# Performance work log

Measured on AMD Instinct MI355X. Metric: run time of the kernel, lower is better.

Reference implementation:

```python
import jax, jax.numpy as jnp
import numpy as np

HEADS = 16
DIM_HEAD = 64
LN_EPS = 1e-5


def _layernorm(x, gamma, beta):
    mu = jnp.mean(x, axis=-1, keepdims=True)
    var = jnp.mean(jnp.square(x - mu), axis=-1, keepdims=True)
    return (x - mu) * jax.lax.rsqrt(var + LN_EPS) * gamma + beta


def setup_inputs() -> dict:
    key = jax.random.key(0)
    k1, k2, k3 = jax.random.split(key, 3)
    B, N, D = 4, 2048, 1024
    inner = HEADS * DIM_HEAD  # 1024
    x = jax.random.normal(k1, (B, N, D), dtype=jnp.float32)
    ln_gamma = jnp.ones((D,), dtype=jnp.float32)
    ln_beta = jnp.zeros((D,), dtype=jnp.float32)
    w_qkv = jax.random.normal(k2, (3 * inner, D), dtype=jnp.float32) * (1.0 / np.sqrt(D))
    w_out = jax.random.normal(k3, (D, inner), dtype=jnp.float32) * (1.0 / np.sqrt(inner))
    b_out = jnp.zeros((D,), dtype=jnp.float32)
    return {"x": x, "ln_gamma": ln_gamma, "ln_beta": ln_beta,
            "w_qkv": w_qkv, "w_out": w_out, "b_out": b_out}


def reference(x, ln_gamma, ln_beta, w_qkv, w_out, b_out):
    B, N, D = x.shape
    h, d = HEADS, DIM_HEAD
    xn = _layernorm(x, ln_gamma, ln_beta)
    qkv = xn @ w_qkv.T  # [B, N, 3*inner]
    q, k, v = jnp.split(qkv, 3, axis=-1)
    q = q.reshape(B, N, h, d)
    k = k.reshape(B, N, h, d)
    v = v.reshape(B, N, h, d)
    scale = 1.0 / np.sqrt(d)  # TET uses 1/sqrt(E); tau=1, delta=0, no mask
    scores = jnp.einsum('blhe,bshe->bhls', q, k)
    A = jax.nn.softmax(scale * scores, axis=-1)  # [B, H, N, N]
    out = jnp.einsum('bhls,bshd->blhd', A, v).reshape(B, N, h * d)
    return out @ w_out.T + b_out
```

## Files before the change

kernel.cpp:

```cpp
#include <hip/hip_runtime.h>

typedef unsigned short ushortT;
typedef __attribute__((ext_vector_type(8))) short short8;
typedef __attribute__((ext_vector_type(4))) float f32x4;

#define QSCALE 0.18033688011112042f

__device__ __forceinline__ ushortT f2bf(float f) {
  union { float f; unsigned int u; } v; v.f = f;
  unsigned int r = v.u + 0x7FFFu + ((v.u >> 16) & 1u);
  return (ushortT)(r >> 16);
}

__device__ __forceinline__ unsigned int pk2bf(float a, float b) {
  union { float f; unsigned int u; } ua, ub; ua.f = a; ub.f = b;
  return __builtin_amdgcn_perm(ub.u + 0x8000u, ua.u + 0x8000u, 0x07060302u);
}

__device__ __forceinline__ void pl_swap(unsigned int& a, unsigned int& b) {
  asm("v_permlane32_swap_b32 %0, %1" : "+v"(a), "+v"(b));
  asm("v_permlane16_swap_b32 %0, %1" : "+v"(a), "+v"(b));
}

__device__ __forceinline__ void gld_lds16(const void* g, void* l) {
  __builtin_amdgcn_global_load_lds(
      (const __attribute__((address_space(1))) unsigned int*)g,
      (__attribute__((address_space(3))) unsigned int*)l, 16, 0, 0);
}

__global__ __launch_bounds__(256) void cvt_kernel(const float* __restrict__ src,
                                                  ushortT* __restrict__ dst, int n4) {
  int i = blockIdx.x * 256 + threadIdx.x;
  if (i < n4) {
    float4 v = ((const float4*)src)[i];
    ushort4 o;
    o.x = f2bf(v.x); o.y = f2bf(v.y); o.z = f2bf(v.z); o.w = f2bf(v.w);
    ((ushort4*)dst)[i] = o;
  }
}

__global__ __launch_bounds__(256) void ln_kernel(const float* __restrict__ x,
                                                 const float* __restrict__ g,
                                                 const float* __restrict__ be,
                                                 ushortT* __restrict__ xn) {
  const int row = blockIdx.x, tid = threadIdx.x;
  const float4 v = ((const float4*)(x + (size_t)row * 1024))[tid];
  float s1 = v.x + v.y + v.z + v.w;
  float s2 = v.x * v.x + v.y * v.y + v.z * v.z + v.w * v.w;
#pragma unroll
  for (int off = 32; off >= 1; off >>= 1) {
    s1 += __shfl_xor(s1, off, 64);
    s2 += __shfl_xor(s2, off, 64);
  }
  __shared__ float red[8];
  const int wave = tid >> 6, lane = tid & 63;
  if (lane == 0) { red[wave] = s1; red[4 + wave] = s2; }
  __syncthreads();
  s1 = red[0] + red[1] + red[2] + red[3];
  s2 = red[4] + red[5] + red[6] + red[7];
  const float mean = s1 * (1.0f / 1024.0f);
  const float var  = s2 * (1.0f / 1024.0f) - mean * mean;
  const float rs = rsqrtf(var + 1e-5f);
  const float4 gv = ((const float4*)g)[tid];
  const float4 bv = ((const float4*)be)[tid];
  ushort4 o;
  o.x = f2bf((v.x - mean) * rs * gv.x + bv.x);
  o.y = f2bf((v.y - mean) * rs * gv.y + bv.y);
  o.z = f2bf((v.z - mean) * rs * gv.z + bv.z);
  o.w = f2bf((v.w - mean) * rs * gv.w + bv.w);
  ((ushort4*)xn)[(size_t)row * 256 + tid] = o;
}

template <int MODE>
__global__ __launch_bounds__(256, 2) void gemm_bt(
    const ushortT* __restrict__ A, const ushortT* __restrict__ Bm,
    int M, int N, int K,
    ushortT* __restrict__ qbuf, ushortT* __restrict__ kbuf, ushortT* __restrict__ vbuf,
    float* __restrict__ outf, const float* __restrict__ bias) {
  __shared__ ushortT lds_a[128 * 64];
  __shared__ ushortT lds_b[128 * 64];
  const int tid = threadIdx.x;
  const int wave = tid >> 6, lane = tid & 63;
  const int q4 = lane >> 4, l16 = lane & 15;
  const int m0 = blockIdx.y * 128, n0 = blockIdx.x * 128;
  const int wm = (wave >> 1) * 64, wn = (wave & 1) * 64;
  const int srow = lane >> 3, scol = (lane & 7) * 8;

  f32x4 acc[4][4];
#pragma unroll
  for (int i = 0; i < 4; i++)
#pragma unroll
    for (int j = 0; j < 4; j++) acc[i][j] = (f32x4){0.f, 0.f, 0.f, 0.f};

  for (int k0 = 0; k0 < K; k0 += 64) {
#pragma unroll
    for (int j = 0; j < 4; j++) {
      const int q = wave * 4 + j;
      gld_lds16(&A[(size_t)(m0 + q * 8 + srow) * K + (k0 + scol)], &lds_a[q * 512]);
      gld_lds16(&Bm[(size_t)(n0 + q * 8 + srow) * K + (k0 + scol)], &lds_b[q * 512]);
    }
    __syncthreads();
#pragma unroll
    for (int kk = 0; kk < 2; kk++) {
      short8 af[4], bf[4];
#pragma unroll
      for (int i = 0; i < 4; i++)
        af[i] = *(const short8*)&lds_a[(wm + i * 16 + l16) * 64 + kk * 32 + q4 * 8];
#pragma unroll
      for (int i = 0; i < 4; i++)
        bf[i] = *(const short8*)&lds_b[(wn + i * 16 + l16) * 64 + kk * 32 + q4 * 8];
#pragma unroll
      for (int im = 0; im < 4; im++)
#pragma unroll
        for (int in = 0; in < 4; in++)
          acc[im][in] = __builtin_amdgcn_mfma_f32_16x16x32_bf16(af[im], bf[in], acc[im][in], 0, 0, 0);
    }
    __syncthreads();
  }

#pragma unroll
  for (int im = 0; im < 4; im++) {
    const int grow_base = m0 + wm + im * 16 + q4 * 4;
#pragma unroll
    for (int in = 0; in < 4; in++) {
      const int c = n0 + wn + in * 16 + l16;
#pragma unroll
      for (int r = 0; r < 4; r++) {
        const float v = acc[im][in][r];
        const int grow = grow_base + r;
        if (MODE == 0) {
          outf[(size_t)grow * N + c] = v + bias[c];
        } else {
          const int which = c >> 10;
          const int h = (c >> 6) & 15;
          const int d = c & 63;
          const int b = grow >> 11, n = grow & 2047;
          if (which == 0) {
            qbuf[((size_t)(b * 16 + h) * 2048 + n) * 64 + d] = f2bf(v * QSCALE);
          } else if (which == 1) {
            kbuf[((size_t)(b * 16 + h) * 2048 + n) * 64 + d] = f2bf(v);
          } else {
            vbuf[((size_t)(b * 16 + h) * 64 + d) * 2048 + n] = f2bf(v);
          }
        }
      }
    }
  }
}

__global__ __launch_bounds__(256, 4) void attn_kernel(
    const ushortT* __restrict__ Qb, const ushortT* __restrict__ Kb,
    const ushortT* __restrict__ Vt, ushortT* __restrict__ Ob) {
  __shared__ ushortT kb[2][4096];
  __shared__ ushortT vb[2][4096];
  const int tid = threadIdx.x;
  const int wave = tid >> 6, lane = tid & 63;
  const int q4 = lane >> 4, l16 = lane & 15;
  const int blk = blockIdx.x;
  const int bh = blk & 63, qt = blk >> 6;
  const ushortT* Qp = Qb + (size_t)bh * (2048 * 64);
  const ushortT* Kp = Kb + (size_t)bh * (2048 * 64);
  const ushortT* Vp = Vt + (size_t)bh * (64 * 2048);
  const int qrow0 = qt * 128 + wave * 32;

  short8 qf[2][2];
#pragma unroll
  for (int qn = 0; qn < 2; qn++)
#pragma unroll
    for (int kk = 0; kk < 2; kk++)
      qf[qn][kk] = *(const short8*)&Qp[(size_t)(qrow0 + qn * 16 + l16) * 64 + kk * 32 + q4 * 8];

  f32x4 acc[4][2];
#pragma unroll
  for (int dn = 0; dn < 4; dn++)
#pragma unroll
    for (int qn = 0; qn < 2; qn++) acc[dn][qn] = (f32x4){0.f, 0.f, 0.f, 0.f};
  float lsum[2] = {0.f, 0.f};

  const int vrow = tid >> 3, vcol = (tid & 7) * 8;
  auto stage = [&](int buf, int s0) {
    gld_lds16(&Kp[(size_t)s0 * 64 + wave * 512 + lane * 8], &kb[buf][wave * 512]);
    gld_lds16(&Kp[(size_t)s0 * 64 + 2048 + wave * 512 + lane * 8], &kb[buf][2048 + wave * 512]);
    gld_lds16(&Vp[(size_t)vrow * 2048 + s0 + vcol], &vb[buf][wave * 512]);
    gld_lds16(&Vp[(size_t)(vrow + 32) * 2048 + s0 + vcol], &vb[buf][2048 + wave * 512]);
  };

  stage(0, 0);

  for (int t = 0; t < 32; t++) {
    const int cur = t & 1;
    __syncthreads();
    if (t < 31) stage(cur ^ 1, (t + 1) * 64);

    f32x4 sa[2][4];
#pragma unroll
    for (int qn = 0; qn < 2; qn++)
#pragma unroll
      for (int cn = 0; cn < 4; cn++) sa[qn][cn] = (f32x4){0.f, 0.f, 0.f, 0.f};
#pragma unroll
    for (int cn = 0; cn < 4; cn++) {
      const short8 kf0 = *(const short8*)&kb[cur][(cn * 16 + l16) * 64 + q4 * 8];
      const short8 kf1 = *(const short8*)&kb[cur][(cn * 16 + l16) * 64 + 32 + q4 * 8];
#pragma unroll
      for (int qn = 0; qn < 2; qn++) {
        sa[qn][cn] = __builtin_amdgcn_mfma_f32_16x16x32_bf16(kf0, qf[qn][0], sa[qn][cn], 0, 0, 0);
        sa[qn][cn] = __builtin_amdgcn_mfma_f32_16x16x32_bf16(kf1, qf[qn][1], sa[qn][cn], 0, 0, 0);
      }
    }

    unsigned int w[2][4][2];
#pragma unroll
    for (int qn = 0; qn < 2; qn++)
#pragma unroll
      for (int cn = 0; cn < 4; cn++) {
        float p0 = __builtin_amdgcn_exp2f(sa[qn][cn][0]);
        float p1 = __builtin_amdgcn_exp2f(sa[qn][cn][1]);
        float p2 = __builtin_amdgcn_exp2f(sa[qn][cn][2]);
        float p3 = __builtin_amdgcn_exp2f(sa[qn][cn][3]);
        lsum[qn] += (p0 + p1) + (p2 + p3);
        w[qn][cn][0] = pk2bf(p0, p1);
        w[qn][cn][1] = pk2bf(p2, p3);
      }

    short8 pf[2][2];
#pragma unroll
    for (int qn = 0; qn < 2; qn++)
#pragma unroll
      for (int ks = 0; ks < 2; ks++) {
        unsigned int a0 = w[qn][2 * ks][0], b0 = w[qn][2 * ks + 1][0];
        unsigned int a1 = w[qn][2 * ks][1], b1 = w[qn][2 * ks + 1][1];
        pl_swap(a0, b0);
        pl_swap(a1, b1);
        union { unsigned int u[4]; short8 s; } tr;
        tr.u[0] = a0; tr.u[1] = a1; tr.u[2] = b0; tr.u[3] = b1;
        pf[qn][ks] = tr.s;
      }

#pragma unroll
    for (int dn = 0; dn < 4; dn++) {
      const short8 vf0 = *(const short8*)&vb[cur][(dn * 16 + l16) * 64 + q4 * 8];
      const short8 vf1 = *(const short8*)&vb[cur][(dn * 16 + l16) * 64 + 32 + q4 * 8];
#pragma unroll
      for (int qn = 0; qn < 2; qn++) {
        acc[dn][qn] = __builtin_amdgcn_mfma_f32_16x16x32_bf16(vf0, pf[qn][0], acc[dn][qn], 0, 0, 0);
        acc[dn][qn] = __builtin_amdgcn_mfma_f32_16x16x32_bf16(vf1, pf[qn][1], acc[dn][qn], 0, 0, 0);
      }
    }
  }

  const int b = bh >> 4, h = bh & 15;
#pragma unroll
  for (int qn = 0; qn < 2; qn++) {
    float l = lsum[qn];
    l += __shfl_xor(l, 16, 64);
    l += __shfl_xor(l, 32, 64);
    const float inv = 1.0f / l;
    const size_t row = (size_t)(b * 2048 + qrow0 + qn * 16 + l16) * 1024 + h * 64;
#pragma unroll
    for (int dn = 0; dn < 4; dn++) {
      ushort4 o;
      o.x = f2bf(acc[dn][qn][0] * inv);
      o.y = f2bf(acc[dn][qn][1] * inv);
      o.z = f2bf(acc[dn][qn][2] * inv);
      o.w = f2bf(acc[dn][qn][3] * inv);
      *(ushort4*)&Ob[row + dn * 16 + q4 * 4] = o;
    }
  }
}

extern "C" void kernel_launch(void* const* d_in, const int* in_sizes, int n_in,
                              void* d_out, int out_size, void* d_ws, size_t ws_size,
                              hipStream_t stream) {
  const float* x    = (const float*)d_in[0];
  const float* g    = (const float*)d_in[1];
  const float* be   = (const float*)d_in[2];
  const float* wqkv = (const float*)d_in[3];
  const float* wout = (const float*)d_in[4];
  const float* bout = (const float*)d_in[5];
  float* out = (float*)d_out;

  char* ws = (char*)d_ws;
  ushortT* xn = (ushortT*)(ws + 0);
  ushortT* wq = (ushortT*)(ws + 16777216);
  ushortT* wo = (ushortT*)(ws + 23068672);
  ushortT* Qb = (ushortT*)(ws + 25165824);
  ushortT* Kb = (ushortT*)(ws + 41943040);
  ushortT* Vt = (ushortT*)(ws + 58720256);
  ushortT* Ob = (ushortT*)(ws + 75497472);

  cvt_kernel<<<3072, 256, 0, stream>>>(wqkv, wq, 786432);
  cvt_kernel<<<1024, 256, 0, stream>>>(wout, wo, 262144);
  ln_kernel<<<8192, 256, 0, stream>>>(x, g, be, xn);
  gemm_bt<1><<<dim3(24, 64), 256, 0, stream>>>(xn, wq, 8192, 3072, 1024,
                                               Qb, Kb, Vt, nullptr, nullptr);
  attn_kernel<<<1024, 256, 0, stream>>>(Qb, Kb, Vt, Ob);
  gemm_bt<0><<<dim3(8, 64), 256, 0, stream>>>(Ob, wo, 8192, 1024, 1024,
                                              nullptr, nullptr, nullptr, out, bout);
}
```

Baseline: 307.4 us.

## Swizzle LDS layouts in GEMM and attention; double query rows per attention block

```diff
diff --git a/kernel.cpp b/kernel.cpp
--- a/kernel.cpp
+++ b/kernel.cpp
@@ -84,7 +84,9 @@
   const int q4 = lane >> 4, l16 = lane & 15;
   const int m0 = blockIdx.y * 128, n0 = blockIdx.x * 128;
   const int wm = (wave >> 1) * 64, wn = (wave & 1) * 64;
-  const int srow = lane >> 3, scol = (lane & 7) * 8;
+  const int srow = lane >> 3;
+  const int scol = ((lane & 7) ^ srow) * 8;
+  const int sw = l16 & 7;
 
   f32x4 acc[4][4];
 #pragma unroll
@@ -105,10 +107,10 @@
       short8 af[4], bf[4];
 #pragma unroll
       for (int i = 0; i < 4; i++)
-        af[i] = *(const short8*)&lds_a[(wm + i * 16 + l16) * 64 + kk * 32 + q4 * 8];
+        af[i] = *(const short8*)&lds_a[(wm + i * 16 + l16) * 64 + ((kk * 4 + q4) ^ sw) * 8];
 #pragma unroll
       for (int i = 0; i < 4; i++)
-        bf[i] = *(const short8*)&lds_b[(wn + i * 16 + l16) * 64 + kk * 32 + q4 * 8];
+        bf[i] = *(const short8*)&lds_b[(wn + i * 16 + l16) * 64 + ((kk * 4 + q4) ^ sw) * 8];
 #pragma unroll
       for (int im = 0; im < 4; im++)
 #pragma unroll
@@ -148,7 +150,7 @@
   }
 }
 
-__global__ __launch_bounds__(256, 4) void attn_kernel(
+__global__ __launch_bounds__(256, 2) void attn_kernel(
     const ushortT* __restrict__ Qb, const ushortT* __restrict__ Kb,
     const ushortT* __restrict__ Vt, ushortT* __restrict__ Ob) {
   __shared__ ushortT kb[2][4096];
@@ -156,33 +158,35 @@
   const int tid = threadIdx.x;
   const int wave = tid >> 6, lane = tid & 63;
   const int q4 = lane >> 4, l16 = lane & 15;
+  const int sw = l16 & 7;
   const int blk = blockIdx.x;
   const int bh = blk & 63, qt = blk >> 6;
   const ushortT* Qp = Qb + (size_t)bh * (2048 * 64);
   const ushortT* Kp = Kb + (size_t)bh * (2048 * 64);
   const ushortT* Vp = Vt + (size_t)bh * (64 * 2048);
-  const int qrow0 = qt * 128 + wave * 32;
-
-  short8 qf[2][2];
-#pragma unroll
-  for (int qn = 0; qn < 2; qn++)
+  const int qrow0 = qt * 256 + wave * 64;
+
+  short8 qf[4][2];
+#pragma unroll
+  for (int qn = 0; qn < 4; qn++)
 #pragma unroll
     for (int kk = 0; kk < 2; kk++)
       qf[qn][kk] = *(const short8*)&Qp[(size_t)(qrow0 + qn * 16 + l16) * 64 + kk * 32 + q4 * 8];
 
-  f32x4 acc[4][2];
+  f32x4 acc[4][4];
 #pragma unroll
   for (int dn = 0; dn < 4; dn++)
 #pragma unroll
-    for (int qn = 0; qn < 2; qn++) acc[dn][qn] = (f32x4){0.f, 0.f, 0.f, 0.f};
-  float lsum[2] = {0.f, 0.f};
-
-  const int vrow = tid >> 3, vcol = (tid & 7) * 8;
+    for (int qn = 0; qn < 4; qn++) acc[dn][qn] = (f32x4){0.f, 0.f, 0.f, 0.f};
+  float lsum[4] = {0.f, 0.f, 0.f, 0.f};
+
+  const int krow = lane >> 3, kchk = ((lane & 7) ^ (lane >> 3)) * 8;
+  const int vrow = tid >> 3, vchk = ((tid & 7) ^ ((tid >> 3) & 7)) * 8;
   auto stage = [&](int buf, int s0) {
-    gld_lds16(&Kp[(size_t)s0 * 64 + wave * 512 + lane * 8], &kb[buf][wave * 512]);
-    gld_lds16(&Kp[(size_t)s0 * 64 + 2048 + wave * 512 + lane * 8], &kb[buf][2048 + wave * 512]);
-    gld_lds16(&Vp[(size_t)vrow * 2048 + s0 + vcol], &vb[buf][wave * 512]);
-    gld_lds16(&Vp[(size_t)(vrow + 32) * 2048 + s0 + vcol], &vb[buf][2048 + wave * 512]);
+    gld_lds16(&Kp[(size_t)(s0 + wave * 8 + krow) * 64 + kchk], &kb[buf][wave * 512]);
+    gld_lds16(&Kp[(size_t)(s0 + 32 + wave * 8 + krow) * 64 + kchk], &kb[buf][2048 + wave * 512]);
+    gld_lds16(&Vp[(size_t)vrow * 2048 + s0 + vchk], &vb[buf][wave * 512]);
+    gld_lds16(&Vp[(size_t)(vrow + 32) * 2048 + s0 + vchk], &vb[buf][2048 + wave * 512]);
   };
 
   stage(0, 0);
@@ -192,25 +196,26 @@
     __syncthreads();
     if (t < 31) stage(cur ^ 1, (t + 1) * 64);
 
-    f32x4 sa[2][4];
-#pragma unroll
-    for (int qn = 0; qn < 2; qn++)
+    f32x4 sa[4][4];
+#pragma unroll
+    for (int qn = 0; qn < 4; qn++)
 #pragma unroll
       for (int cn = 0; cn < 4; cn++) sa[qn][cn] = (f32x4){0.f, 0.f, 0.f, 0.f};
 #pragma unroll
     for (int cn = 0; cn < 4; cn++) {
-      const short8 kf0 = *(const short8*)&kb[cur][(cn * 16 + l16) * 64 + q4 * 8];
-      const short8 kf1 = *(const short8*)&kb[cur][(cn * 16 + l16) * 64 + 32 + q4 * 8];
-#pragma unroll
-      for (int qn = 0; qn < 2; qn++) {
+      const short8 kf0 = *(const short8*)&kb[cur][(cn * 16 + l16) * 64 + (q4 ^ sw) * 8];
+      const short8 kf1 = *(const short8*)&kb[cur][(cn * 16 + l16) * 64 + ((q4 + 4) ^ sw) * 8];
+#pragma unroll
+      for (int qn = 0; qn < 4; qn++) {
         sa[qn][cn] = __builtin_amdgcn_mfma_f32_16x16x32_bf16(kf0, qf[qn][0], sa[qn][cn], 0, 0, 0);
         sa[qn][cn] = __builtin_amdgcn_mfma_f32_16x16x32_bf16(kf1, qf[qn][1], sa[qn][cn], 0, 0, 0);
       }
     }
 
-    unsigned int w[2][4][2];
-#pragma unroll
-    for (int qn = 0; qn < 2; qn++)
+    short8 pf[4][2];
+#pragma unroll
+    for (int qn = 0; qn < 4; qn++) {
+      unsigned int w[4][2];
 #pragma unroll
       for (int cn = 0; cn < 4; cn++) {
         float p0 = __builtin_amdgcn_exp2f(sa[qn][cn][0]);
@@ -218,30 +223,27 @@
         float p2 = __builtin_amdgcn_exp2f(sa[qn][cn][2]);
         float p3 = __builtin_amdgcn_exp2f(sa[qn][cn][3]);
         lsum[qn] += (p0 + p1) + (p2 + p3);
-        w[qn][cn][0] = pk2bf(p0, p1);
-        w[qn][cn][1] = pk2bf(p2, p3);
-      }
-
-    short8 pf[2][2];
-#pragma unroll
-    for (int qn = 0; qn < 2; qn++)
+        w[cn][0] = pk2bf(p0, p1);
+        w[cn][1] = pk2bf(p2, p3);
+      }
 #pragma unroll
       for (int ks = 0; ks < 2; ks++) {
-        unsigned int a0 = w[qn][2 * ks][0], b0 = w[qn][2 * ks + 1][0];
-        unsigned int a1 = w[qn][2 * ks][1], b1 = w[qn][2 * ks + 1][1];
+        unsigned int a0 = w[2 * ks][0], b0 = w[2 * ks + 1][0];
+        unsigned int a1 = w[2 * ks][1], b1 = w[2 * ks + 1][1];
         pl_swap(a0, b0);
         pl_swap(a1, b1);
         union { unsigned int u[4]; short8 s; } tr;
         tr.u[0] = a0; tr.u[1] = a1; tr.u[2] = b0; tr.u[3] = b1;
         pf[qn][ks] = tr.s;
       }
+    }
 
 #pragma unroll
     for (int dn = 0; dn < 4; dn++) {
-      const short8 vf0 = *(const short8*)&vb[cur][(dn * 16 + l16) * 64 + q4 * 8];
-      const short8 vf1 = *(const short8*)&vb[cur][(dn * 16 + l16) * 64 + 32 + q4 * 8];
-#pragma unroll
-      for (int qn = 0; qn < 2; qn++) {
+      const short8 vf0 = *(const short8*)&vb[cur][(dn * 16 + l16) * 64 + (q4 ^ sw) * 8];
+      const short8 vf1 = *(const short8*)&vb[cur][(dn * 16 + l16) * 64 + ((q4 + 4) ^ sw) * 8];
+#pragma unroll
+      for (int qn = 0; qn < 4; qn++) {
         acc[dn][qn] = __builtin_amdgcn_mfma_f32_16x16x32_bf16(vf0, pf[qn][0], acc[dn][qn], 0, 0, 0);
         acc[dn][qn] = __builtin_amdgcn_mfma_f32_16x16x32_bf16(vf1, pf[qn][1], acc[dn][qn], 0, 0, 0);
       }
@@ -250,7 +252,7 @@
 
   const int b = bh >> 4, h = bh & 15;
 #pragma unroll
-  for (int qn = 0; qn < 2; qn++) {
+  for (int qn = 0; qn < 4; qn++) {
     float l = lsum[qn];
     l += __shfl_xor(l, 16, 64);
     l += __shfl_xor(l, 32, 64);
@@ -293,7 +295,7 @@
   ln_kernel<<<8192, 256, 0, stream>>>(x, g, be, xn);
   gemm_bt<1><<<dim3(24, 64), 256, 0, stream>>>(xn, wq, 8192, 3072, 1024,
                                                Qb, Kb, Vt, nullptr, nullptr);
-  attn_kernel<<<1024, 256, 0, stream>>>(Qb, Kb, Vt, Ob);
+  attn_kernel<<<512, 256, 0, stream>>>(Qb, Kb, Vt, Ob);
   gemm_bt<0><<<dim3(8, 64), 256, 0, stream>>>(Ob, wo, 8192, 1024, 1024,
                                               nullptr, nullptr, nullptr, out, bout);
 }
```

Result: faster. 300.3 us (-2.3%).
